# Kernel tuning notes

Measured on AMD Instinct MI355X. Metric: run time of the kernel, lower is better.

The kernel has to match this reference:

```python
import jax, jax.numpy as jnp
import numpy as np

N = 50000          # num nodes
IN_DIM = 256       # input feature dim
OUT_DIM = 64       # output dim
SUPPORT = 8        # num relations
NUM_BASES = 4
NNZ = 800000       # nonzeros in sparse A [N, SUPPORT*N]


def setup_inputs() -> dict:
    key = jax.random.key(0)
    ks = jax.random.split(key, 6)
    E = jax.random.normal(ks[0], (N, IN_DIM), dtype=jnp.float32)
    W_F = jax.random.normal(ks[1], (NUM_BASES, IN_DIM, OUT_DIM), dtype=jnp.float32) * 0.05
    W_F_comp = jax.random.normal(ks[2], (SUPPORT, NUM_BASES), dtype=jnp.float32)
    b = jnp.zeros((OUT_DIM,), dtype=jnp.float32)
    A_vals = jax.random.uniform(ks[3], (NNZ,), dtype=jnp.float32)
    A_rows = jax.random.randint(ks[4], (NNZ,), 0, N, dtype=jnp.int32)
    A_cols = jax.random.randint(ks[5], (NNZ,), 0, SUPPORT * N, dtype=jnp.int32)
    return {"E": E, "W_F": W_F, "W_F_comp": W_F_comp, "b": b,
            "A_vals": A_vals, "A_rows": A_rows, "A_cols": A_cols}


def reference(E, W_F, W_F_comp, b, A_vals, A_rows, A_cols):
    # Basis decomposition: per-relation weights W[s] = sum_b comp[s,b] * W_F[b]
    # (matches transpose/einsum/transpose chain in the original call())
    W = jnp.einsum('sb,bio->sio', W_F_comp, W_F)          # [S, in, out]
    # Dense feature transform per relation, then flatten relation blocks
    FW = jnp.einsum('ni,sio->sno', E, W)                  # [S, N, out]
    FW = FW.reshape(SUPPORT * N, OUT_DIM)                 # [S*N, out]
    # Sparse A [N, S*N] @ FW  (tf.sparse_tensor_dense_matmul)
    msgs = A_vals[:, None] * FW[A_cols]                   # [nnz, out] gather
    AXW = jax.ops.segment_sum(msgs, A_rows, num_segments=N)  # [N, out] scatter-add
    return jax.nn.relu(AXW + b)
```

## Files before the change

### kernel.cpp

```cpp
#include <hip/hip_runtime.h>
#include <hip/hip_bf16.h>

typedef unsigned int  uint32;
typedef __attribute__((ext_vector_type(8))) short short8;
typedef __attribute__((ext_vector_type(4))) float f32x4;

#define NNODES   50000
#define IN_DIM   256
#define OUT_DIM  64
#define SUPPORT  8
#define NUM_BASES 4
#define NNZ      800000

#define M_PAD    50048
#define NBIG     512
#define CAP      48

#define GEMM_BLOCKS 1564
#define FILL_BLOCKS 512
#define MEGA_BLOCKS 2076
#define CAST_BLOCKS 6256
#define CW_BLOCKS   (CAST_BLOCKS + NBIG)

#define EBF_OFF  0u
#define WT_OFF   25624576u
#define FW_OFF   25886720u
#define CNT_OFF  77086720u
#define BK_OFF   77286720u

__device__ __forceinline__ unsigned short f2bf_rne(float f) {
    uint32 u = __float_as_uint(f);
    u = (u + 0x7fffu + ((u >> 16) & 1u)) >> 16;
    return (unsigned short)u;
}
__device__ __forceinline__ float bf2f(unsigned short b) {
    return __uint_as_float(((uint32)b) << 16);
}
__device__ __forceinline__ void load_lds16(const void* g, void* l) {
    __builtin_amdgcn_global_load_lds(
        (const __attribute__((address_space(1))) void*)g,
        (__attribute__((address_space(3))) void*)l, 16, 0, 0);
}

__global__ __launch_bounds__(256) void cast_wbig_kernel(
    const float* __restrict__ E, unsigned short* __restrict__ Ebf,
    const float* __restrict__ WF, const float* __restrict__ comp,
    unsigned short* __restrict__ WT)
{
    const int bid = blockIdx.x;
    const int tid = threadIdx.x;

    if (bid >= CAST_BLOCKS) {
        const int n = bid - CAST_BLOCKS;
        const int k = tid;
        const int o = n & 63, s = n >> 6;
        float v = 0.f;
        #pragma unroll
        for (int b = 0; b < NUM_BASES; ++b)
            v = fmaf(comp[s * 4 + b], WF[(b * IN_DIM + k) * OUT_DIM + o], v);
        WT[n * IN_DIM + k] = f2bf_rne(v);
        return;
    }

    const int i8 = bid * 256 + tid;
    unsigned short o[8];
    if (i8 < NNODES * IN_DIM / 8) {
        const float4 f0 = reinterpret_cast<const float4*>(E)[i8 * 2];
        const float4 f1 = reinterpret_cast<const float4*>(E)[i8 * 2 + 1];
        o[0]=f2bf_rne(f0.x); o[1]=f2bf_rne(f0.y); o[2]=f2bf_rne(f0.z); o[3]=f2bf_rne(f0.w);
        o[4]=f2bf_rne(f1.x); o[5]=f2bf_rne(f1.y); o[6]=f2bf_rne(f1.z); o[7]=f2bf_rne(f1.w);
    } else {
        #pragma unroll
        for (int j = 0; j < 8; ++j) o[j] = 0;
    }
    reinterpret_cast<ulonglong2*>(Ebf)[i8] = *reinterpret_cast<ulonglong2*>(o);
}

__global__ __launch_bounds__(256) void mega_kernel(
    const unsigned short* __restrict__ Ebf,
    const unsigned short* __restrict__ WT,
    unsigned short* __restrict__ FW,
    const float* __restrict__ vals, const int* __restrict__ rows,
    const int* __restrict__ cols, int* __restrict__ cnt,
    int2* __restrict__ bucket)
{
    __shared__ short Alds[128 * 64];
    __shared__ short Blds[128 * 64];

    const int bid = blockIdx.x;
    const int tid = threadIdx.x;

    int g;
    if (bid < 2048) {
        if ((bid & 3) == 3) {
            for (int e = (bid >> 2) * 256 + tid; e < NNZ; e += FILL_BLOCKS * 256) {
                const int r = rows[e];
                const int p = atomicAdd(&cnt[r], 1);
                if (p < CAP)
                    bucket[(size_t)r * CAP + p] =
                        make_int2(cols[e], __float_as_int(vals[e]));
            }
            return;
        }
        g = 3 * (bid >> 2) + (bid & 3);
    } else {
        g = 1536 + (bid - 2048);
    }

    const int lane = tid & 63;
    const int wid  = tid >> 6;
    const int wr   = wid >> 1;
    const int wc   = wid & 1;
    const int m0   = (g % 391) * 128;
    const int n0   = (g / 391) * 128;

    f32x4 acc[4][4];
    #pragma unroll
    for (int i = 0; i < 4; ++i)
        #pragma unroll
        for (int j = 0; j < 4; ++j) acc[i][j] = (f32x4){0.f, 0.f, 0.f, 0.f};

    const int srow = lane >> 3;
    const int scol = (lane & 7) * 16;

    for (int kt = 0; kt < 4; ++kt) {
        #pragma unroll
        for (int i = 0; i < 4; ++i) {
            const int c   = wid * 4 + i;
            const int row = c * 8 + srow;
            load_lds16(
                (const char*)Ebf + (size_t)(m0 + row) * 512 + kt * 128 + scol,
                (char*)Alds + c * 1024);
            load_lds16(
                (const char*)WT + (size_t)(n0 + row) * 512 + kt * 128 + scol,
                (char*)Blds + c * 1024);
        }
        __syncthreads();

        #pragma unroll
        for (int ks = 0; ks < 2; ++ks) {
            short8 af[4], bf[4];
            const int k0 = ks * 32 + (lane >> 4) * 8;
            #pragma unroll
            for (int mi = 0; mi < 4; ++mi)
                af[mi] = *reinterpret_cast<const short8*>(
                    &Alds[(wr * 64 + mi * 16 + (lane & 15)) * 64 + k0]);
            #pragma unroll
            for (int ni = 0; ni < 4; ++ni)
                bf[ni] = *reinterpret_cast<const short8*>(
                    &Blds[(wc * 64 + ni * 16 + (lane & 15)) * 64 + k0]);
            #pragma unroll
            for (int mi = 0; mi < 4; ++mi)
                #pragma unroll
                for (int ni = 0; ni < 4; ++ni)
                    acc[mi][ni] = __builtin_amdgcn_mfma_f32_16x16x32_bf16(
                        af[mi], bf[ni], acc[mi][ni], 0, 0, 0);
        }
        __syncthreads();
    }

    #pragma unroll
    for (int mi = 0; mi < 4; ++mi) {
        #pragma unroll
        for (int r = 0; r < 4; ++r) {
            const int row = m0 + wr * 64 + mi * 16 + (lane >> 4) * 4 + r;
            if (row < NNODES) {
                #pragma unroll
                for (int ni = 0; ni < 4; ++ni) {
                    const int col = n0 + wc * 64 + ni * 16 + (lane & 15);
                    FW[((size_t)(col >> 6) * NNODES + row) * 64 + (col & 63)]
                        = f2bf_rne(acc[mi][ni][r]);
                }
            }
        }
    }
}

__global__ __launch_bounds__(256) void scatter_csr_kernel(
    const int* __restrict__ cnt, const int2* __restrict__ bucket,
    const unsigned short* __restrict__ FW, const float* __restrict__ bias,
    float* __restrict__ out)
{
    const int lane = threadIdx.x & 63;
    const int r    = blockIdx.x * 4 + (threadIdx.x >> 6);
    if (r >= NNODES) return;

    const int n = min(cnt[r], CAP);
    int2 my = make_int2(0, 0);
    if (lane < CAP) my = bucket[(size_t)r * CAP + lane];

    float a0 = 0.f, a1 = 0.f, a2 = 0.f, a3 = 0.f;
    int j = 0;
    for (; j + 4 <= n; j += 4) {
        const uint32 c0 = (uint32)__builtin_amdgcn_readlane(my.x, j);
        const uint32 c1 = (uint32)__builtin_amdgcn_readlane(my.x, j + 1);
        const uint32 c2 = (uint32)__builtin_amdgcn_readlane(my.x, j + 2);
        const uint32 c3 = (uint32)__builtin_amdgcn_readlane(my.x, j + 3);
        const float  v0 = __int_as_float(__builtin_amdgcn_readlane(my.y, j));
        const float  v1 = __int_as_float(__builtin_amdgcn_readlane(my.y, j + 1));
        const float  v2 = __int_as_float(__builtin_amdgcn_readlane(my.y, j + 2));
        const float  v3 = __int_as_float(__builtin_amdgcn_readlane(my.y, j + 3));
        const unsigned short f0 = FW[(size_t)c0 * 64 + lane];
        const unsigned short f1 = FW[(size_t)c1 * 64 + lane];
        const unsigned short f2 = FW[(size_t)c2 * 64 + lane];
        const unsigned short f3 = FW[(size_t)c3 * 64 + lane];
        a0 = fmaf(v0, bf2f(f0), a0);
        a1 = fmaf(v1, bf2f(f1), a1);
        a2 = fmaf(v2, bf2f(f2), a2);
        a3 = fmaf(v3, bf2f(f3), a3);
    }
    for (; j < n; ++j) {
        const uint32 c = (uint32)__builtin_amdgcn_readlane(my.x, j);
        const float  v = __int_as_float(__builtin_amdgcn_readlane(my.y, j));
        a0 = fmaf(v, bf2f(FW[(size_t)c * 64 + lane]), a0);
    }
    const float acc = (a0 + a1) + (a2 + a3);
    out[(size_t)r * OUT_DIM + lane] = fmaxf(acc + bias[lane], 0.f);
}

extern "C" void kernel_launch(void* const* d_in, const int* in_sizes, int n_in,
                              void* d_out, int out_size, void* d_ws, size_t ws_size,
                              hipStream_t stream) {
    const float* E     = (const float*)d_in[0];
    const float* WF    = (const float*)d_in[1];
    const float* comp  = (const float*)d_in[2];
    const float* b     = (const float*)d_in[3];
    const float* Avals = (const float*)d_in[4];
    const int*   Arows = (const int*)d_in[5];
    const int*   Acols = (const int*)d_in[6];
    float* out = (float*)d_out;

    char* ws = (char*)d_ws;
    unsigned short* Ebf = (unsigned short*)(ws + EBF_OFF);
    unsigned short* WT  = (unsigned short*)(ws + WT_OFF);
    unsigned short* FW  = (unsigned short*)(ws + FW_OFF);
    int*   cnt    = (int*)(ws + CNT_OFF);
    int2*  bucket = (int2*)(ws + BK_OFF);

    hipMemsetAsync(cnt, 0, NNODES * sizeof(int), stream);

    cast_wbig_kernel<<<CW_BLOCKS, 256, 0, stream>>>(E, Ebf, WF, comp, WT);

    mega_kernel<<<MEGA_BLOCKS, 256, 0, stream>>>(
        Ebf, WT, FW, Avals, Arows, Acols, cnt, bucket);

    scatter_csr_kernel<<<(NNODES + 3) / 4, 256, 0, stream>>>(
        cnt, bucket, FW, b, out);
}
```

Before: 220.4 us.

## Replace global-atomic bucket fill with two-pass LDS binning and XOR-swizzled GEMM tiles

Drops the global-atomic per-row bucket fill that was fused into the GEMM kernel and the cnt memset. In their place it adds a two-pass scheme: a bin kernel groups edges into 64-row bins per input chunk using LDS atomics, and a scatter kernel prefix-scans and counting-sorts each bin in LDS before the per-row gather. It also XOR-swizzles the GEMM's LDS tile layout to avoid bank conflicts, and reuses the Ebf workspace region for binned edges after the GEMM finishes. The risks are that capacity caps (SEGCAP 32 per chunk-bin, RAWCAP 1536 per bin) may drop edges, and that binning now runs serially after the GEMM instead of overlapping it.

```diff
diff --git a/kernel.cpp b/kernel.cpp
--- a/kernel.cpp
+++ b/kernel.cpp
@@ -14,19 +14,20 @@
 
 #define M_PAD    50048
 #define NBIG     512
-#define CAP      48
-
-#define GEMM_BLOCKS 1564
-#define FILL_BLOCKS 512
-#define MEGA_BLOCKS 2076
 #define CAST_BLOCKS 6256
 #define CW_BLOCKS   (CAST_BLOCKS + NBIG)
 
+#define NBINS    782
+#define P1_BLOCKS 128
+#define EPB      6250
+#define SEGCAP   32
+#define RAWCAP   1536
+
 #define EBF_OFF  0u
+#define BIN_OFF  0u
 #define WT_OFF   25624576u
 #define FW_OFF   25886720u
-#define CNT_OFF  77086720u
-#define BK_OFF   77286720u
+#define BC_OFF   77086720u
 
 __device__ __forceinline__ unsigned short f2bf_rne(float f) {
     uint32 u = __float_as_uint(f);
@@ -76,43 +77,21 @@
     reinterpret_cast<ulonglong2*>(Ebf)[i8] = *reinterpret_cast<ulonglong2*>(o);
 }
 
-__global__ __launch_bounds__(256) void mega_kernel(
+__global__ __launch_bounds__(256) void gemm_kernel(
     const unsigned short* __restrict__ Ebf,
     const unsigned short* __restrict__ WT,
-    unsigned short* __restrict__ FW,
-    const float* __restrict__ vals, const int* __restrict__ rows,
-    const int* __restrict__ cols, int* __restrict__ cnt,
-    int2* __restrict__ bucket)
+    unsigned short* __restrict__ FW)
 {
     __shared__ short Alds[128 * 64];
     __shared__ short Blds[128 * 64];
 
-    const int bid = blockIdx.x;
-    const int tid = threadIdx.x;
-
-    int g;
-    if (bid < 2048) {
-        if ((bid & 3) == 3) {
-            for (int e = (bid >> 2) * 256 + tid; e < NNZ; e += FILL_BLOCKS * 256) {
-                const int r = rows[e];
-                const int p = atomicAdd(&cnt[r], 1);
-                if (p < CAP)
-                    bucket[(size_t)r * CAP + p] =
-                        make_int2(cols[e], __float_as_int(vals[e]));
-            }
-            return;
-        }
-        g = 3 * (bid >> 2) + (bid & 3);
-    } else {
-        g = 1536 + (bid - 2048);
-    }
-
+    const int tid  = threadIdx.x;
     const int lane = tid & 63;
     const int wid  = tid >> 6;
     const int wr   = wid >> 1;
     const int wc   = wid & 1;
-    const int m0   = (g % 391) * 128;
-    const int n0   = (g / 391) * 128;
+    const int m0   = blockIdx.x * 128;
+    const int n0   = blockIdx.y * 128;
 
     f32x4 acc[4][4];
     #pragma unroll
@@ -120,8 +99,8 @@
         #pragma unroll
         for (int j = 0; j < 4; ++j) acc[i][j] = (f32x4){0.f, 0.f, 0.f, 0.f};
 
-    const int srow = lane >> 3;
-    const int scol = (lane & 7) * 16;
+    const int srow    = lane >> 3;
+    const int scol_sw = ((lane & 7) ^ srow) << 4;
 
     for (int kt = 0; kt < 4; ++kt) {
         #pragma unroll
@@ -129,10 +108,10 @@
             const int c   = wid * 4 + i;
             const int row = c * 8 + srow;
             load_lds16(
-                (const char*)Ebf + (size_t)(m0 + row) * 512 + kt * 128 + scol,
+                (const char*)Ebf + (size_t)(m0 + row) * 512 + kt * 128 + scol_sw,
                 (char*)Alds + c * 1024);
             load_lds16(
-                (const char*)WT + (size_t)(n0 + row) * 512 + kt * 128 + scol,
+                (const char*)WT + (size_t)(n0 + row) * 512 + kt * 128 + scol_sw,
                 (char*)Blds + c * 1024);
         }
         __syncthreads();
@@ -140,15 +119,15 @@
         #pragma unroll
         for (int ks = 0; ks < 2; ++ks) {
             short8 af[4], bf[4];
-            const int k0 = ks * 32 + (lane >> 4) * 8;
+            const int sa = (((ks * 4 + (lane >> 4)) ^ (lane & 7)) << 3);
             #pragma unroll
             for (int mi = 0; mi < 4; ++mi)
                 af[mi] = *reinterpret_cast<const short8*>(
-                    &Alds[(wr * 64 + mi * 16 + (lane & 15)) * 64 + k0]);
+                    &Alds[(wr * 64 + mi * 16 + (lane & 15)) * 64 + sa]);
             #pragma unroll
             for (int ni = 0; ni < 4; ++ni)
                 bf[ni] = *reinterpret_cast<const short8*>(
-                    &Blds[(wc * 64 + ni * 16 + (lane & 15)) * 64 + k0]);
+                    &Blds[(wc * 64 + ni * 16 + (lane & 15)) * 64 + sa]);
             #pragma unroll
             for (int mi = 0; mi < 4; ++mi)
                 #pragma unroll
@@ -176,46 +155,126 @@
     }
 }
 
-__global__ __launch_bounds__(256) void scatter_csr_kernel(
-    const int* __restrict__ cnt, const int2* __restrict__ bucket,
+__global__ __launch_bounds__(256) void bin_kernel(
+    const float* __restrict__ vals, const int* __restrict__ rows,
+    const int* __restrict__ cols, int* __restrict__ bcnt,
+    int2* __restrict__ binned)
+{
+    __shared__ int cur[NBINS];
+    const int tid = threadIdx.x, bid = blockIdx.x;
+    for (int i = tid; i < NBINS; i += 256) cur[i] = 0;
+    __syncthreads();
+
+    const int base = bid * EPB;
+    for (int i = tid; i < EPB; i += 256) {
+        const int e = base + i;
+        const int r = rows[e];
+        const int c = cols[e];
+        const int v = __float_as_int(vals[e]);
+        const int b = r >> 6;
+        const int p = atomicAdd(&cur[b], 1);
+        if (p < SEGCAP)
+            binned[(size_t)(bid * NBINS + b) * SEGCAP + p] =
+                make_int2(((r & 63) << 19) | c, v);
+    }
+    __syncthreads();
+    for (int i = tid; i < NBINS; i += 256)
+        bcnt[bid * NBINS + i] = min(cur[i], SEGCAP);
+}
+
+__global__ __launch_bounds__(256) void bin_scatter_kernel(
+    const int* __restrict__ bcnt, const int2* __restrict__ binned,
     const unsigned short* __restrict__ FW, const float* __restrict__ bias,
     float* __restrict__ out)
 {
-    const int lane = threadIdx.x & 63;
-    const int r    = blockIdx.x * 4 + (threadIdx.x >> 6);
-    if (r >= NNODES) return;
-
-    const int n = min(cnt[r], CAP);
-    int2 my = make_int2(0, 0);
-    if (lane < CAP) my = bucket[(size_t)r * CAP + lane];
-
-    float a0 = 0.f, a1 = 0.f, a2 = 0.f, a3 = 0.f;
-    int j = 0;
-    for (; j + 4 <= n; j += 4) {
-        const uint32 c0 = (uint32)__builtin_amdgcn_readlane(my.x, j);
-        const uint32 c1 = (uint32)__builtin_amdgcn_readlane(my.x, j + 1);
-        const uint32 c2 = (uint32)__builtin_amdgcn_readlane(my.x, j + 2);
-        const uint32 c3 = (uint32)__builtin_amdgcn_readlane(my.x, j + 3);
-        const float  v0 = __int_as_float(__builtin_amdgcn_readlane(my.y, j));
-        const float  v1 = __int_as_float(__builtin_amdgcn_readlane(my.y, j + 1));
-        const float  v2 = __int_as_float(__builtin_amdgcn_readlane(my.y, j + 2));
-        const float  v3 = __int_as_float(__builtin_amdgcn_readlane(my.y, j + 3));
-        const unsigned short f0 = FW[(size_t)c0 * 64 + lane];
-        const unsigned short f1 = FW[(size_t)c1 * 64 + lane];
-        const unsigned short f2 = FW[(size_t)c2 * 64 + lane];
-        const unsigned short f3 = FW[(size_t)c3 * 64 + lane];
-        a0 = fmaf(v0, bf2f(f0), a0);
-        a1 = fmaf(v1, bf2f(f1), a1);
-        a2 = fmaf(v2, bf2f(f2), a2);
-        a3 = fmaf(v3, bf2f(f3), a3);
-    }
-    for (; j < n; ++j) {
-        const uint32 c = (uint32)__builtin_amdgcn_readlane(my.x, j);
-        const float  v = __int_as_float(__builtin_amdgcn_readlane(my.y, j));
-        a0 = fmaf(v, bf2f(FW[(size_t)c * 64 + lane]), a0);
-    }
-    const float acc = (a0 + a1) + (a2 + a3);
-    out[(size_t)r * OUT_DIM + lane] = fmaxf(acc + bias[lane], 0.f);
+    __shared__ int2 raw[RAWCAP];
+    __shared__ int2 srt[RAWCAP];
+    __shared__ int  sscan[P1_BLOCKS];
+    __shared__ int  seg_off[P1_BLOCKS + 1];
+    __shared__ int  hscan[64];
+    __shared__ int  row_off[65];
+    __shared__ int  cur[64];
+
+    const int tid  = threadIdx.x;
+    const int beta = blockIdx.x;
+
+    if (tid < P1_BLOCKS) sscan[tid] = bcnt[tid * NBINS + beta];
+    __syncthreads();
+    for (int off = 1; off < P1_BLOCKS; off <<= 1) {
+        int v = 0;
+        if (tid < P1_BLOCKS && tid >= off) v = sscan[tid - off];
+        __syncthreads();
+        if (tid < P1_BLOCKS) sscan[tid] += v;
+        __syncthreads();
+    }
+    if (tid < P1_BLOCKS) seg_off[tid + 1] = sscan[tid];
+    if (tid == 0) seg_off[0] = 0;
+    __syncthreads();
+    const int T = min(seg_off[P1_BLOCKS], RAWCAP);
+
+    for (int i = tid; i < T; i += 256) {
+        int lo = 0, hi = P1_BLOCKS - 1;
+        while (lo < hi) {
+            const int mid = (lo + hi + 1) >> 1;
+            if (seg_off[mid] <= i) lo = mid; else hi = mid - 1;
+        }
+        raw[i] = binned[(size_t)(lo * NBINS + beta) * SEGCAP + (i - seg_off[lo])];
+    }
+    if (tid < 64) hscan[tid] = 0;
+    __syncthreads();
+    for (int i = tid; i < T; i += 256)
+        atomicAdd(&hscan[raw[i].x >> 19], 1);
+    __syncthreads();
+    for (int off = 1; off < 64; off <<= 1) {
+        int v = 0;
+        if (tid < 64 && tid >= off) v = hscan[tid - off];
+        __syncthreads();
+        if (tid < 64) hscan[tid] += v;
+        __syncthreads();
+    }
+    if (tid < 64) row_off[tid + 1] = hscan[tid];
+    if (tid == 0) row_off[0] = 0;
+    __syncthreads();
+    if (tid < 64) cur[tid] = row_off[tid];
+    __syncthreads();
+    for (int i = tid; i < T; i += 256) {
+        const int rl = raw[i].x >> 19;
+        const int p  = atomicAdd(&cur[rl], 1);
+        srt[p] = make_int2(raw[i].x & 0x7FFFF, raw[i].y);
+    }
+    __syncthreads();
+
+    const int lane = tid & 63;
+    const int w    = tid >> 6;
+    const float bl = bias[lane];
+    for (int rl = w; rl < 64; rl += 4) {
+        const int r = (beta << 6) + rl;
+        if (r >= NNODES) break;
+        const int lo = row_off[rl];
+        const int n  = row_off[rl + 1] - lo;
+        float a0 = 0.f, a1 = 0.f, a2 = 0.f, a3 = 0.f;
+        int j = 0;
+        for (; j + 4 <= n; j += 4) {
+            const int2 e0 = srt[lo + j];
+            const int2 e1 = srt[lo + j + 1];
+            const int2 e2 = srt[lo + j + 2];
+            const int2 e3 = srt[lo + j + 3];
+            const unsigned short f0 = FW[(size_t)e0.x * 64 + lane];
+            const unsigned short f1 = FW[(size_t)e1.x * 64 + lane];
+            const unsigned short f2 = FW[(size_t)e2.x * 64 + lane];
+            const unsigned short f3 = FW[(size_t)e3.x * 64 + lane];
+            a0 = fmaf(__int_as_float(e0.y), bf2f(f0), a0);
+            a1 = fmaf(__int_as_float(e1.y), bf2f(f1), a1);
+            a2 = fmaf(__int_as_float(e2.y), bf2f(f2), a2);
+            a3 = fmaf(__int_as_float(e3.y), bf2f(f3), a3);
+        }
+        for (; j < n; ++j) {
+            const int2 e = srt[lo + j];
+            a0 = fmaf(__int_as_float(e.y), bf2f(FW[(size_t)e.x * 64 + lane]), a0);
+        }
+        const float acc = (a0 + a1) + (a2 + a3);
+        out[(size_t)r * OUT_DIM + lane] = fmaxf(acc + bl, 0.f);
+    }
 }
 
 extern "C" void kernel_launch(void* const* d_in, const int* in_sizes, int n_in,
@@ -231,19 +290,17 @@
     float* out = (float*)d_out;
 
     char* ws = (char*)d_ws;
-    unsigned short* Ebf = (unsigned short*)(ws + EBF_OFF);
-    unsigned short* WT  = (unsigned short*)(ws + WT_OFF);
-    unsigned short* FW  = (unsigned short*)(ws + FW_OFF);
-    int*   cnt    = (int*)(ws + CNT_OFF);
-    int2*  bucket = (int2*)(ws + BK_OFF);
-
-    hipMemsetAsync(cnt, 0, NNODES * sizeof(int), stream);
+    unsigned short* Ebf    = (unsigned short*)(ws + EBF_OFF);
+    unsigned short* WT     = (unsigned short*)(ws + WT_OFF);
+    unsigned short* FW     = (unsigned short*)(ws + FW_OFF);
+    int*            bcnt   = (int*)(ws + BC_OFF);
+    int2*           binned = (int2*)(ws + BIN_OFF);
 
     cast_wbig_kernel<<<CW_BLOCKS, 256, 0, stream>>>(E, Ebf, WF, comp, WT);
 
-    mega_kernel<<<MEGA_BLOCKS, 256, 0, stream>>>(
-        Ebf, WT, FW, Avals, Arows, Acols, cnt, bucket);
-
-    scatter_csr_kernel<<<(NNODES + 3) / 4, 256, 0, stream>>>(
-        cnt, bucket, FW, b, out);
-}
+    gemm_kernel<<<dim3(M_PAD / 128, NBIG / 128), 256, 0, stream>>>(Ebf, WT, FW);
+
+    bin_kernel<<<P1_BLOCKS, 256, 0, stream>>>(Avals, Arows, Acols, bcnt, binned);
+
+    bin_scatter_kernel<<<NBINS, 256, 0, stream>>>(bcnt, binned, FW, b, out);
+}
```

Result: faster. 210.0 us (-4.7%).
